# Optimization experiments

Hardware: AMD Instinct MI355X
Metric: run time of the kernel (lower is better)

Reference implementation:

```python
import jax, jax.numpy as jnp
import numpy as np

N_NODES = 1_000_000
N_EDGES = 32_000_000
EPS_INIT = 100.0


def setup_inputs() -> dict:
    key = jax.random.key(0)
    ks = jax.random.split(key, 8)
    x = jax.random.normal(ks[0], (N_NODES, 1), dtype=jnp.float32)
    edge_index = jax.random.randint(ks[1], (2, N_EDGES), 0, N_NODES, dtype=jnp.int64)
    # MLP params: Linear(1,20) -> ReLU -> Linear(20,20) -> ReLU -> Linear(20,1)
    w1 = jax.random.normal(ks[2], (1, 20), dtype=jnp.float32) / np.sqrt(1.0)
    b1 = jnp.zeros((20,), dtype=jnp.float32)
    w2 = jax.random.normal(ks[3], (20, 20), dtype=jnp.float32) / np.sqrt(20.0)
    b2 = jnp.zeros((20,), dtype=jnp.float32)
    w3 = jax.random.normal(ks[4], (20, 1), dtype=jnp.float32) / np.sqrt(20.0)
    b3 = jnp.zeros((1,), dtype=jnp.float32)
    eps = jnp.asarray(EPS_INIT, dtype=jnp.float32)
    return {"x": x, "edge_index": edge_index, "eps": eps,
            "w1": w1, "b1": b1, "w2": w2, "b2": b2, "w3": w3, "b3": b3}


def reference(x, edge_index, eps, w1, b1, w2, b2, w3, b3):
    # GINConv: out = MLP((1 + eps) * x + sum_{j in N(i)} x_j)
    src, dst = edge_index[0], edge_index[1]
    # gather source features per edge, scatter-add to destination nodes
    agg = jax.ops.segment_sum(x[src], dst, num_segments=N_NODES)  # [N, 1]
    h = (1.0 + eps) * x + agg
    h = jax.nn.relu(h @ w1 + b1)   # [N, 20]
    h = jax.nn.relu(h @ w2 + b2)   # [N, 20]
    out = h @ w3 + b3              # [N, 1]
    return out
```

## Files before the change

### kernel.cpp

```cpp
#include <hip/hip_runtime.h>

#define N_NODES 1000000
#define N_EDGES 32000000

#define NB        256
#define TSC       1024
#define EPB       125000
#define QPB       31250
#define NBKT      245
#define BKT_PAD   256
#define CAP       135168
#define RING      96
#define RSTRIDE   97
#define QSIZE     1024

#define QSCALE    32768.0f
#define QINV      (1.0f / 32768.0f)

#define BINS_ELEMS  ((size_t)NBKT * CAP)
#define CNT_ELEMS   ((size_t)NB * BKT_PAD)
#define PAGG_ELEMS  ((size_t)NBKT * 2 * 4096)
#define WS_NEEDED   ((BINS_ELEMS + CNT_ELEMS + BKT_PAD + PAGG_ELEMS) * 4)

typedef int  iv4 __attribute__((ext_vector_type(4)));
typedef unsigned uv4 __attribute__((ext_vector_type(4)));


__global__ __launch_bounds__(TSC) void gin_count(const int* __restrict__ dst,
                                                 unsigned* __restrict__ cnt) {
    __shared__ unsigned h[BKT_PAD];
    int tid = threadIdx.x;
    if (tid < BKT_PAD) h[tid] = 0u;
    __syncthreads();
    int k = blockIdx.x;
    const iv4* q = reinterpret_cast<const iv4*>(dst) + (size_t)k * QPB;
    for (int base = 0; base < QPB; base += TSC * 4) {
        int i0 = base + tid, i1 = i0 + TSC, i2 = i1 + TSC, i3 = i2 + TSC;
        iv4 d0 = {0,0,0,0}, d1 = {0,0,0,0}, d2 = {0,0,0,0}, d3 = {0,0,0,0};
        bool v0 = i0 < QPB, v1 = i1 < QPB, v2 = i2 < QPB, v3 = i3 < QPB;
        if (v0) d0 = __builtin_nontemporal_load(&q[i0]);
        if (v1) d1 = __builtin_nontemporal_load(&q[i1]);
        if (v2) d2 = __builtin_nontemporal_load(&q[i2]);
        if (v3) d3 = __builtin_nontemporal_load(&q[i3]);
        if (v0) { atomicAdd(&h[d0.x >> 12], 1u); atomicAdd(&h[d0.y >> 12], 1u);
                  atomicAdd(&h[d0.z >> 12], 1u); atomicAdd(&h[d0.w >> 12], 1u); }
        if (v1) { atomicAdd(&h[d1.x >> 12], 1u); atomicAdd(&h[d1.y >> 12], 1u);
                  atomicAdd(&h[d1.z >> 12], 1u); atomicAdd(&h[d1.w >> 12], 1u); }
        if (v2) { atomicAdd(&h[d2.x >> 12], 1u); atomicAdd(&h[d2.y >> 12], 1u);
                  atomicAdd(&h[d2.z >> 12], 1u); atomicAdd(&h[d2.w >> 12], 1u); }
        if (v3) { atomicAdd(&h[d3.x >> 12], 1u); atomicAdd(&h[d3.y >> 12], 1u);
                  atomicAdd(&h[d3.z >> 12], 1u); atomicAdd(&h[d3.w >> 12], 1u); }
    }
    __syncthreads();
    if (tid < BKT_PAD) cnt[(size_t)k * BKT_PAD + tid] = h[tid];
}

__global__ void gin_scan(unsigned* __restrict__ cnt, unsigned* __restrict__ tot) {
    int gtid = blockIdx.x * blockDim.x + threadIdx.x;
    int b = gtid >> 6;
    int lane = gtid & 63;
    if (b >= BKT_PAD) return;
    unsigned running = 0;
    for (int base = 0; base < NB; base += 64) {
        int idx = base + lane;
        unsigned v = (idx < NB) ? cnt[(size_t)idx * BKT_PAD + b] : 0u;
        unsigned s = v;
        for (int d = 1; d < 64; d <<= 1) {
            unsigned u = __shfl_up(s, d);
            if (lane >= d) s += u;
        }
        unsigned excl = s - v;
        if (idx < NB) cnt[(size_t)idx * BKT_PAD + b] = running + excl;
        running += __shfl(s, 63);
    }
    if (lane == 0) tot[b] = running;
}

__global__ __launch_bounds__(TSC) void gin_scatter_bins(const int* __restrict__ src,
                                                        const int* __restrict__ dst,
                                                        const float* __restrict__ x,
                                                        const unsigned* __restrict__ cnt,
                                                        unsigned* __restrict__ bins) {
    __shared__ unsigned stage[BKT_PAD][RSTRIDE];
    __shared__ unsigned stot[BKT_PAD];
    __shared__ unsigned sflt[BKT_PAD];
    __shared__ unsigned sbase[BKT_PAD];
    __shared__ unsigned queue[QSIZE];
    __shared__ unsigned qcount;

    int tid = threadIdx.x;
    int k = blockIdx.x;
    if (tid < BKT_PAD) {
        stot[tid] = 0u;
        sflt[tid] = 0u;
        sbase[tid] = cnt[(size_t)k * BKT_PAD + tid];
    }
    if (tid == 0) qcount = 0;
    __syncthreads();

    const iv4* qs = reinterpret_cast<const iv4*>(src) + (size_t)k * QPB;
    const iv4* qd = reinterpret_cast<const iv4*>(dst) + (size_t)k * QPB;

#define QUANT(xx) ((unsigned)__float2int_rn((xx) * QSCALE) & 0xFFFFFu)

    iv4 s_n1 = {0,0,0,0}, d_cur = {0,0,0,0}, d_n1 = {0,0,0,0};
    unsigned qc0 = 0, qc1 = 0, qc2 = 0, qc3 = 0;
    bool v_cur = tid < QPB;
    bool v_n1 = tid + TSC < QPB;
    {
        iv4 s0 = {0,0,0,0};
        if (v_cur) {
            s0 = __builtin_nontemporal_load(&qs[tid]);
            d_cur = __builtin_nontemporal_load(&qd[tid]);
        }
        if (v_n1) {
            s_n1 = __builtin_nontemporal_load(&qs[tid + TSC]);
            d_n1 = __builtin_nontemporal_load(&qd[tid + TSC]);
        }
        if (v_cur) {
            qc0 = QUANT(x[s0.x]); qc1 = QUANT(x[s0.y]);
            qc2 = QUANT(x[s0.z]); qc3 = QUANT(x[s0.w]);
        }
    }

    for (int t0 = 0; t0 < QPB; t0 += TSC) {
        int i2 = t0 + 2 * TSC + tid;
        iv4 s_n2 = {0,0,0,0}, d_n2 = {0,0,0,0};
        bool v_n2 = i2 < QPB;
        if (v_n2) {
            s_n2 = __builtin_nontemporal_load(&qs[i2]);
            d_n2 = __builtin_nontemporal_load(&qd[i2]);
        }
        unsigned qn0 = 0, qn1 = 0, qn2 = 0, qn3 = 0;
        if (v_n1) {
            qn0 = QUANT(x[s_n1.x]); qn1 = QUANT(x[s_n1.y]);
            qn2 = QUANT(x[s_n1.z]); qn3 = QUANT(x[s_n1.w]);
        }

        if (tid == 0) qcount = 0;
        if (v_cur) {
#define PUT(qq, dd) do {                                                     \
            unsigned b_ = (unsigned)(dd) >> 12;                              \
            unsigned p_ = atomicAdd(&stot[b_], 1u);                          \
            stage[b_][p_ % RING] =                                           \
                (((unsigned)(dd) & 4095u) << 20) | (qq);                     \
        } while (0)
            PUT(qc0, d_cur.x);
            PUT(qc1, d_cur.y);
            PUT(qc2, d_cur.z);
            PUT(qc3, d_cur.w);
#undef PUT
        }
        __syncthreads();
        if (tid < BKT_PAD) {
            unsigned T = stot[tid], F = sflt[tid];
            unsigned nch = (T - F) >> 5;
            if (nch) {
                unsigned off = atomicAdd(&qcount, nch);
                for (unsigned c = 0; c < nch; ++c)
                    queue[off + c] = ((unsigned)tid << 3) | c;
            }
        }
        __syncthreads();
        {
            unsigned C = qcount;
            unsigned lane = tid & 31;
            for (unsigned g = tid >> 5; g < C; g += TSC / 32) {
                unsigned qe = queue[g];
                unsigned b = qe >> 3, c = qe & 7;
                unsigned pos = sflt[b] + (c << 5) + lane;
                unsigned gp = sbase[b] + pos;
                if (gp < CAP)
                    __builtin_nontemporal_store(stage[b][pos % RING],
                                                &bins[(size_t)b * CAP + gp]);
            }
        }
        __syncthreads();
        if (tid < BKT_PAD) {
            unsigned T = stot[tid], F = sflt[tid];
            sflt[tid] = F + (((T - F) >> 5) << 5);
        }
        qc0 = qn0; qc1 = qn1; qc2 = qn2; qc3 = qn3;
        d_cur = d_n1; v_cur = v_n1;
        s_n1 = s_n2; d_n1 = d_n2; v_n1 = v_n2;
    }
#undef QUANT
    __syncthreads();
    if (tid < BKT_PAD) {
        unsigned b = (unsigned)tid;
        unsigned T = stot[b];
        unsigned F = sflt[b];
        unsigned gbase = sbase[b];
        unsigned* gout = bins + (size_t)b * CAP;
        for (; F < T; ++F) {
            unsigned gp = gbase + F;
            if (gp < CAP) gout[gp] = stage[b][F % RING];
        }
    }
}

__global__ __launch_bounds__(1024) void gin_reduce(const unsigned* __restrict__ bins,
                                                   const unsigned* __restrict__ tot,
                                                   float* __restrict__ pagg) {
    __shared__ int acc[4096];
    int tid = threadIdx.x;
    int blk = blockIdx.x;
    int b = blk >> 1;
    int h = blk & 1;
    for (int i = tid; i < 4096; i += 1024) acc[i] = 0;
    __syncthreads();

    unsigned n = tot[b];
    if (n > CAP) n = CAP;
    const unsigned* bb = bins + (size_t)b * CAP;
    const uv4* bb4 = reinterpret_cast<const uv4*>(bb);
    unsigned nq = n >> 2;
    unsigned q_lo = h ? (nq >> 1) : 0;
    unsigned q_hi = h ? nq : (nq >> 1);

#define DEC(u) atomicAdd(&acc[(u) >> 20], ((int)((u) << 12)) >> 12)
    for (unsigned i = q_lo + tid; i < q_hi; i += 1024) {
        uv4 e = __builtin_nontemporal_load(&bb4[i]);
        DEC(e.x); DEC(e.y); DEC(e.z); DEC(e.w);
    }
    if (h) {
        for (unsigned j = (nq << 2) + tid; j < n; j += 1024) {
            unsigned e = __builtin_nontemporal_load(&bb[j]);
            DEC(e);
        }
    }
#undef DEC
    __syncthreads();

    float* po = pagg + (size_t)blk * 4096;
    for (int j = tid; j < 4096; j += 1024) po[j] = (float)acc[j] * QINV;
}

__global__ __launch_bounds__(512) void gin_combine_mlp(const float* __restrict__ pagg,
                               const float* __restrict__ x,
                               const float* __restrict__ eps,
                               const float* __restrict__ w1,
                               const float* __restrict__ b1,
                               const float* __restrict__ w2,
                               const float* __restrict__ b2,
                               const float* __restrict__ w3,
                               const float* __restrict__ b3,
                               float* __restrict__ out) {
    int i = blockIdx.x * blockDim.x + threadIdx.x;
    if (i >= N_NODES) return;
    int b = i >> 12;
    int j = i & 4095;
    float agg = pagg[(size_t)(b * 2) * 4096 + j] + pagg[(size_t)(b * 2 + 1) * 4096 + j];
    float h0 = (1.0f + eps[0]) * x[i] + agg;

    float h1[20];
#pragma unroll
    for (int jj = 0; jj < 20; ++jj)
        h1[jj] = fmaxf(fmaf(h0, w1[jj], b1[jj]), 0.0f);

    float o = b3[0];
#pragma unroll
    for (int kk = 0; kk < 20; ++kk) {
        float a = b2[kk];
#pragma unroll
        for (int jj = 0; jj < 20; ++jj)
            a = fmaf(h1[jj], w2[jj * 20 + kk], a);
        o = fmaf(fmaxf(a, 0.0f), w3[kk], o);
    }
    out[i] = o;
}

__global__ void gin_zero_kernel(float* __restrict__ agg, int n) {
    int i = blockIdx.x * blockDim.x + threadIdx.x;
    if (i < n) agg[i] = 0.0f;
}

__global__ void gin_scatter_kernel(const float* __restrict__ x,
                                   const int* __restrict__ src,
                                   const int* __restrict__ dst,
                                   float* __restrict__ agg) {
    int q = blockIdx.x * blockDim.x + threadIdx.x;
    int e = q * 4;
    if (e + 3 < N_EDGES) {
        int4 s = *reinterpret_cast<const int4*>(src + e);
        int4 d = *reinterpret_cast<const int4*>(dst + e);
        atomicAdd(&agg[d.x], x[s.x]);
        atomicAdd(&agg[d.y], x[s.y]);
        atomicAdd(&agg[d.z], x[s.z]);
        atomicAdd(&agg[d.w], x[s.w]);
    } else if (e < N_EDGES) {
        for (; e < N_EDGES; ++e) atomicAdd(&agg[dst[e]], x[src[e]]);
    }
}

__global__ void gin_mlp_kernel(const float* __restrict__ x,
                               const float* __restrict__ agg,
                               const float* __restrict__ eps,
                               const float* __restrict__ w1,
                               const float* __restrict__ b1,
                               const float* __restrict__ w2,
                               const float* __restrict__ b2,
                               const float* __restrict__ w3,
                               const float* __restrict__ b3,
                               float* __restrict__ out) {
    int i = blockIdx.x * blockDim.x + threadIdx.x;
    if (i >= N_NODES) return;
    float h0 = (1.0f + eps[0]) * x[i] + agg[i];
    float h1[20];
#pragma unroll
    for (int j = 0; j < 20; ++j) h1[j] = fmaxf(fmaf(h0, w1[j], b1[j]), 0.0f);
    float o = b3[0];
#pragma unroll
    for (int k = 0; k < 20; ++k) {
        float a = b2[k];
#pragma unroll
        for (int j = 0; j < 20; ++j) a = fmaf(h1[j], w2[j * 20 + k], a);
        o = fmaf(fmaxf(a, 0.0f), w3[k], o);
    }
    out[i] = o;
}

extern "C" void kernel_launch(void* const* d_in, const int* in_sizes, int n_in,
                              void* d_out, int out_size, void* d_ws, size_t ws_size,
                              hipStream_t stream) {
    const float* x    = (const float*)d_in[0];
    const int*   ei   = (const int*)  d_in[1];
    const float* eps  = (const float*)d_in[2];
    const float* w1   = (const float*)d_in[3];
    const float* b1   = (const float*)d_in[4];
    const float* w2   = (const float*)d_in[5];
    const float* b2   = (const float*)d_in[6];
    const float* w3   = (const float*)d_in[7];
    const float* b3   = (const float*)d_in[8];
    float* out = (float*)d_out;

    const int* src = ei;
    const int* dst = ei + N_EDGES;

    if (ws_size >= WS_NEEDED) {
        unsigned* bins = (unsigned*)d_ws;
        unsigned* cnt  = bins + BINS_ELEMS;
        unsigned* tot  = cnt + CNT_ELEMS;
        float*    pagg = (float*)(tot + BKT_PAD);

        gin_count<<<NB, TSC, 0, stream>>>(dst, cnt);
        {
            int blocks = (BKT_PAD * 64 + 255) / 256;
            gin_scan<<<blocks, 256, 0, stream>>>(cnt, tot);
        }
        gin_scatter_bins<<<NB, TSC, 0, stream>>>(src, dst, x, cnt, bins);
        gin_reduce<<<NBKT * 2, 1024, 0, stream>>>(bins, tot, pagg);
        gin_combine_mlp<<<(N_NODES + 511) / 512, 512, 0, stream>>>(pagg, x, eps,
                                                 w1, b1, w2, b2, w3, b3, out);
    } else {
        float* agg = (ws_size >= (size_t)N_NODES * sizeof(float)) ? (float*)d_ws : out;
        {
            int blocks = (N_NODES + 255) / 256;
            gin_zero_kernel<<<blocks, 256, 0, stream>>>(agg, N_NODES);
        }
        {
            int quads = N_EDGES / 4;
            int blocks = (quads + 255) / 256;
            gin_scatter_kernel<<<blocks, 256, 0, stream>>>(x, src, dst, agg);
        }
        {
            int blocks = (N_NODES + 255) / 256;
            gin_mlp_kernel<<<blocks, 256, 0, stream>>>(x, agg, eps, w1, b1, w2, b2,
                                                       w3, b3, out);
        }
    }
}
```

Measured before the change: 399.7 us.

## Warp-specialize scatter kernel: gather warps prefetch quantized x into LDS double buffer

Splits each 1024-thread block in the bin-scatter kernel into two halves. The upper 512 threads gather and quantize x[src] for the next tile into a double-buffered LDS array, while the lower 512 threads load dst and push the current tile's entries into the bucket staging ring. The aim is to overlap the latency of the random x gathers with the LDS atomic binning, replacing the old register-level software pipeline. The cost is extra LDS (32 KB), which may lower occupancy, and only half the threads doing each job, so each half handles twice as many items per tile.

```diff
diff --git a/kernel.cpp b/kernel.cpp
--- a/kernel.cpp
+++ b/kernel.cpp
@@ -5,7 +5,6 @@
 
 #define NB        256
 #define TSC       1024
-#define EPB       125000
 #define QPB       31250
 #define NBKT      245
 #define BKT_PAD   256
@@ -13,6 +12,8 @@
 #define RING      96
 #define RSTRIDE   97
 #define QSIZE     1024
+#define TQ        1024
+#define NT        ((QPB + TQ - 1) / TQ)
 
 #define QSCALE    32768.0f
 #define QINV      (1.0f / 32768.0f)
@@ -76,12 +77,13 @@
     if (lane == 0) tot[b] = running;
 }
 
-__global__ __launch_bounds__(TSC) void gin_scatter_bins(const int* __restrict__ src,
-                                                        const int* __restrict__ dst,
-                                                        const float* __restrict__ x,
-                                                        const unsigned* __restrict__ cnt,
-                                                        unsigned* __restrict__ bins) {
+__global__ __launch_bounds__(TSC) void gin_scatter_fused(const int* __restrict__ src,
+                                                         const int* __restrict__ dst,
+                                                         const float* __restrict__ x,
+                                                         const unsigned* __restrict__ cnt,
+                                                         unsigned* __restrict__ bins) {
     __shared__ unsigned stage[BKT_PAD][RSTRIDE];
+    __shared__ unsigned qv[2][TQ * 4];
     __shared__ unsigned stot[BKT_PAD];
     __shared__ unsigned sflt[BKT_PAD];
     __shared__ unsigned sbase[BKT_PAD];
@@ -96,60 +98,70 @@
         sbase[tid] = cnt[(size_t)k * BKT_PAD + tid];
     }
     if (tid == 0) qcount = 0;
-    __syncthreads();
 
     const iv4* qs = reinterpret_cast<const iv4*>(src) + (size_t)k * QPB;
     const iv4* qd = reinterpret_cast<const iv4*>(dst) + (size_t)k * QPB;
 
 #define QUANT(xx) ((unsigned)__float2int_rn((xx) * QSCALE) & 0xFFFFFu)
 
-    iv4 s_n1 = {0,0,0,0}, d_cur = {0,0,0,0}, d_n1 = {0,0,0,0};
-    unsigned qc0 = 0, qc1 = 0, qc2 = 0, qc3 = 0;
-    bool v_cur = tid < QPB;
-    bool v_n1 = tid + TSC < QPB;
-    {
-        iv4 s0 = {0,0,0,0};
-        if (v_cur) {
-            s0 = __builtin_nontemporal_load(&qs[tid]);
-            d_cur = __builtin_nontemporal_load(&qd[tid]);
-        }
-        if (v_n1) {
-            s_n1 = __builtin_nontemporal_load(&qs[tid + TSC]);
-            d_n1 = __builtin_nontemporal_load(&qd[tid + TSC]);
-        }
-        if (v_cur) {
-            qc0 = QUANT(x[s0.x]); qc1 = QUANT(x[s0.y]);
-            qc2 = QUANT(x[s0.z]); qc3 = QUANT(x[s0.w]);
-        }
-    }
-
-    for (int t0 = 0; t0 < QPB; t0 += TSC) {
-        int i2 = t0 + 2 * TSC + tid;
-        iv4 s_n2 = {0,0,0,0}, d_n2 = {0,0,0,0};
-        bool v_n2 = i2 < QPB;
-        if (v_n2) {
-            s_n2 = __builtin_nontemporal_load(&qs[i2]);
-            d_n2 = __builtin_nontemporal_load(&qd[i2]);
-        }
-        unsigned qn0 = 0, qn1 = 0, qn2 = 0, qn3 = 0;
-        if (v_n1) {
-            qn0 = QUANT(x[s_n1.x]); qn1 = QUANT(x[s_n1.y]);
-            qn2 = QUANT(x[s_n1.z]); qn3 = QUANT(x[s_n1.w]);
-        }
-
+    bool isGW = tid >= 512;
+    int g = tid & 511;
+
+    if (isGW) {
+#pragma unroll
+        for (int r = 0; r < 2; ++r) {
+            int qit = g + r * 512;
+            int q = qit;
+            if (q < QPB) {
+                iv4 s4 = __builtin_nontemporal_load(&qs[q]);
+                qv[0][qit * 4 + 0] = QUANT(x[s4.x]);
+                qv[0][qit * 4 + 1] = QUANT(x[s4.y]);
+                qv[0][qit * 4 + 2] = QUANT(x[s4.z]);
+                qv[0][qit * 4 + 3] = QUANT(x[s4.w]);
+            }
+        }
+    }
+    __syncthreads();
+
+    for (int t = 0; t < NT; ++t) {
+        int cur = t & 1, nxt = cur ^ 1;
         if (tid == 0) qcount = 0;
-        if (v_cur) {
+        if (isGW) {
+            int t1 = t + 1;
+            if (t1 < NT) {
+#pragma unroll
+                for (int r = 0; r < 2; ++r) {
+                    int qit = g + r * 512;
+                    int q = t1 * TQ + qit;
+                    if (q < QPB) {
+                        iv4 s4 = __builtin_nontemporal_load(&qs[q]);
+                        qv[nxt][qit * 4 + 0] = QUANT(x[s4.x]);
+                        qv[nxt][qit * 4 + 1] = QUANT(x[s4.y]);
+                        qv[nxt][qit * 4 + 2] = QUANT(x[s4.z]);
+                        qv[nxt][qit * 4 + 3] = QUANT(x[s4.w]);
+                    }
+                }
+            }
+        } else {
+#pragma unroll
+            for (int r = 0; r < 2; ++r) {
+                int qit = g + r * 512;
+                int q = t * TQ + qit;
+                if (q < QPB) {
+                    iv4 d4 = __builtin_nontemporal_load(&qd[q]);
 #define PUT(qq, dd) do {                                                     \
-            unsigned b_ = (unsigned)(dd) >> 12;                              \
-            unsigned p_ = atomicAdd(&stot[b_], 1u);                          \
-            stage[b_][p_ % RING] =                                           \
-                (((unsigned)(dd) & 4095u) << 20) | (qq);                     \
-        } while (0)
-            PUT(qc0, d_cur.x);
-            PUT(qc1, d_cur.y);
-            PUT(qc2, d_cur.z);
-            PUT(qc3, d_cur.w);
+                    unsigned b_ = (unsigned)(dd) >> 12;                      \
+                    unsigned p_ = atomicAdd(&stot[b_], 1u);                  \
+                    stage[b_][p_ % RING] =                                   \
+                        (((unsigned)(dd) & 4095u) << 20) | (qq);             \
+                } while (0)
+                    PUT(qv[cur][qit * 4 + 0], d4.x);
+                    PUT(qv[cur][qit * 4 + 1], d4.y);
+                    PUT(qv[cur][qit * 4 + 2], d4.z);
+                    PUT(qv[cur][qit * 4 + 3], d4.w);
 #undef PUT
+                }
+            }
         }
         __syncthreads();
         if (tid < BKT_PAD) {
@@ -165,8 +177,8 @@
         {
             unsigned C = qcount;
             unsigned lane = tid & 31;
-            for (unsigned g = tid >> 5; g < C; g += TSC / 32) {
-                unsigned qe = queue[g];
+            for (unsigned gg = tid >> 5; gg < C; gg += TSC / 32) {
+                unsigned qe = queue[gg];
                 unsigned b = qe >> 3, c = qe & 7;
                 unsigned pos = sflt[b] + (c << 5) + lane;
                 unsigned gp = sbase[b] + pos;
@@ -180,9 +192,6 @@
             unsigned T = stot[tid], F = sflt[tid];
             sflt[tid] = F + (((T - F) >> 5) << 5);
         }
-        qc0 = qn0; qc1 = qn1; qc2 = qn2; qc3 = qn3;
-        d_cur = d_n1; v_cur = v_n1;
-        s_n1 = s_n2; d_n1 = d_n2; v_n1 = v_n2;
     }
 #undef QUANT
     __syncthreads();
@@ -348,7 +357,7 @@
             int blocks = (BKT_PAD * 64 + 255) / 256;
             gin_scan<<<blocks, 256, 0, stream>>>(cnt, tot);
         }
-        gin_scatter_bins<<<NB, TSC, 0, stream>>>(src, dst, x, cnt, bins);
+        gin_scatter_fused<<<NB, TSC, 0, stream>>>(src, dst, x, cnt, bins);
         gin_reduce<<<NBKT * 2, 1024, 0, stream>>>(bins, tot, pagg);
         gin_combine_mlp<<<(N_NODES + 511) / 512, 512, 0, stream>>>(pagg, x, eps,
                                                  w1, b1, w2, b2, w3, b3, out);
```

Result: slower. 412.6 us (+3.2%).
